# Performance work log

Measured on AMD Instinct MI355X. Metric: run time of the kernel, lower is better.

Reference implementation:

```python
import jax, jax.numpy as jnp
import numpy as np

NEG = -1e30


def _layernorm(x, g, b, eps=1e-6):
    mu = jnp.mean(x, axis=-1, keepdims=True)
    var = jnp.mean((x - mu) ** 2, axis=-1, keepdims=True)
    return (x - mu) * jax.lax.rsqrt(var + eps) * g + b


def _ctc_loss(log_probs, targets, input_lengths, target_lengths, blank):
    # log_probs: (T, B, V); targets: (B, L) int; lengths: (B,) int
    T, B, V = log_probs.shape
    L = targets.shape[1]
    S = 2 * L + 1
    # extended target sequence: blank, t0, blank, t1, ..., blank
    ext = jnp.full((B, S), blank, dtype=targets.dtype)
    ext = ext.at[:, 1::2].set(targets)
    # skip transition allowed where label differs from label two back and is not blank
    ext_m2 = jnp.pad(ext, ((0, 0), (2, 0)), constant_values=blank)[:, :S]
    skip_mask = (jnp.arange(S)[None, :] >= 2) & (ext != ext_m2) & (ext != blank)
    # gather per-step emission log-probs for extended labels: (T, B, S)
    lp_ext = jnp.take_along_axis(
        log_probs, jnp.broadcast_to(ext[None], (T, B, S)), axis=2
    )

    alpha0 = jnp.full((B, S), NEG, dtype=log_probs.dtype)
    alpha0 = alpha0.at[:, 0].set(lp_ext[0, :, 0])
    alpha0 = alpha0.at[:, 1].set(lp_ext[0, :, 1])

    def step(alpha, lp_e):
        a1 = jnp.pad(alpha, ((0, 0), (1, 0)), constant_values=NEG)[:, :S]
        a2 = jnp.pad(alpha, ((0, 0), (2, 0)), constant_values=NEG)[:, :S]
        a2 = jnp.where(skip_mask, a2, NEG)
        new = jnp.logaddexp(jnp.logaddexp(alpha, a1), a2) + lp_e
        return new, new

    _, alphas_rest = jax.lax.scan(step, alpha0, lp_ext[1:])
    alphas = jnp.concatenate([alpha0[None], alphas_rest], axis=0)  # (T, B, S)

    alpha_T = alphas[input_lengths - 1, jnp.arange(B)]  # (B, S)
    s_end = 2 * target_lengths  # final blank position
    l_blank = jnp.take_along_axis(alpha_T, s_end[:, None], axis=1)[:, 0]
    l_label = jnp.take_along_axis(alpha_T, (s_end - 1)[:, None], axis=1)[:, 0]
    loss_b = -jnp.logaddexp(l_blank, l_label)
    # zero_infinity=True
    loss_b = jnp.where(loss_b > 1e29, 0.0, loss_b)
    # reduction='mean': divide each loss by its target length, then batch-mean
    return jnp.mean(loss_b / target_lengths.astype(loss_b.dtype))


def setup_inputs() -> dict:
    T, B, D, V, L = 2000, 32, 768, 1024, 150
    key = jax.random.key(0)
    ks = jax.random.split(key, 8)
    s = 0.02
    return {
        "source_encoder_output": jax.random.normal(ks[0], (T, B, D), jnp.float32),
        "W_proj": jax.random.normal(ks[1], (D, D), jnp.float32) * s,
        "b_proj": jnp.zeros((D,), jnp.float32),
        "W_tr": jax.random.normal(ks[2], (D, D), jnp.float32) * s,
        "b_tr": jnp.zeros((D,), jnp.float32),
        "ln_g": jnp.ones((D,), jnp.float32),
        "ln_b": jnp.zeros((D,), jnp.float32),
        "W_dec": jax.random.normal(ks[3], (D, V), jnp.float32) * s,
        "b_dec": jnp.zeros((V,), jnp.float32),
        "target_syllabe_ids": jax.random.randint(ks[4], (B, L), 1, V, jnp.int32),
        "source_encoder_output_lengths": jnp.full((B,), T, jnp.int32),
        "target_syllabe_id_lengths": jnp.full((B,), L, jnp.int32),
    }


def reference(source_encoder_output, W_proj, b_proj, W_tr, b_tr, ln_g, ln_b,
              W_dec, b_dec, target_syllabe_ids, source_encoder_output_lengths,
              target_syllabe_id_lengths):
    BLANK = 0
    x = source_encoder_output @ W_proj + b_proj          # encoder_projection
    x = jax.nn.gelu(x @ W_tr + b_tr, approximate=False)  # transform dense + gelu
    x = _layernorm(x, ln_g, ln_b, eps=1e-6)
    scores = x @ W_dec + b_dec                           # acoustic_decoder
    log_probs = jax.nn.log_softmax(scores, axis=-1)      # (T, B, V)
    return _ctc_loss(log_probs, target_syllabe_ids,
                     source_encoder_output_lengths,
                     target_syllabe_id_lengths, BLANK)
```

## Files before the change

### kernel.cpp

```cpp
#include <hip/hip_runtime.h>
#include <hip/hip_bf16.h>
#include <math.h>
#include <stdint.h>

#define NEGF (-1e30f)
#define LOG2E 1.44269504088896340736f
#define LN2 0.69314718055994530942f

#define LPROW 512

typedef short bf16x8 __attribute__((ext_vector_type(8)));
typedef float f32x4 __attribute__((ext_vector_type(4)));

__device__ __forceinline__ unsigned short f2b(float x) {
  __hip_bfloat16 h = __float2bfloat16(x);
  return *reinterpret_cast<unsigned short*>(&h);
}
__device__ __forceinline__ float b2f(unsigned short u) {
  __hip_bfloat16 h;
  *reinterpret_cast<unsigned short*>(&h) = u;
  return __bfloat162float(h);
}
__device__ __forceinline__ float gelu_exact(float x) {
  return 0.5f * x * (1.0f + erff(x * 0.70710678118654752440f));
}

#if __has_builtin(__builtin_amdgcn_logf)
__device__ __forceinline__ float fast_log2(float x) { return __builtin_amdgcn_logf(x); }
#else
__device__ __forceinline__ float fast_log2(float x) { return log2f(x); }
#endif

template<int CTRL>
__device__ __forceinline__ float dpp_shr(float x) {
  return __int_as_float(__builtin_amdgcn_update_dpp(
      0, __float_as_int(x), 0x110 | CTRL, 0xf, 0xf, true));
}
__device__ __forceinline__ float readlane_f(float x, int l) {
  return __int_as_float(__builtin_amdgcn_readlane(__float_as_int(x), l));
}

__device__ __forceinline__ void gload16(void* lds, const void* g) {
  __builtin_amdgcn_global_load_lds(
      (__attribute__((address_space(1))) void*)(uintptr_t)g,
      (__attribute__((address_space(3))) void*)(unsigned int)(uintptr_t)lds,
      16, 0, 0);
}

__global__ __launch_bounds__(256) void cvt_enc_kernel(
    const float* __restrict__ in, unsigned short* __restrict__ out, long n4)
{
  long i = (long)blockIdx.x * blockDim.x + threadIdx.x;
  const long stride = (long)gridDim.x * blockDim.x;
  for (; i < n4; i += stride) {
    float4 v = ((const float4*)in)[i];
    ushort4 o;
    o.x = f2b(v.x); o.y = f2b(v.y); o.z = f2b(v.z); o.w = f2b(v.w);
    ((ushort4*)out)[i] = o;
  }
}

__global__ __launch_bounds__(256) void cvt_wt_kernel(
    const float* __restrict__ W, unsigned short* __restrict__ WT, int K, int N)
{
  __shared__ float tile[32][33];
  const int n0 = blockIdx.x * 32, k0 = blockIdx.y * 32;
  const int tx = threadIdx.x, ty = threadIdx.y;
#pragma unroll
  for (int i = 0; i < 32; i += 8) {
    int k = k0 + ty + i, n = n0 + tx;
    tile[ty + i][tx] = (k < K && n < N) ? W[(long)k * N + n] : 0.f;
  }
  __syncthreads();
#pragma unroll
  for (int i = 0; i < 32; i += 8) {
    int n = n0 + ty + i, k = k0 + tx;
    if (n < N && k < K) WT[(long)n * K + k] = f2b(tile[tx][ty + i]);
  }
}

template<int NFULL, int EPI>
__global__ __launch_bounds__(256, 2) void gemm128_kernel(
    const unsigned short* __restrict__ A,
    const unsigned short* __restrict__ WT,
    const float* __restrict__ bias,
    unsigned short* __restrict__ out,
    float2* __restrict__ partials,
    int K)
{
  extern __shared__ char smem[];
  unsigned short* As = (unsigned short*)smem;
  unsigned short* Bs = (unsigned short*)(smem + 16384);

  const int tid = threadIdx.x, lane = tid & 63, w = tid >> 6;
  const int wr = w >> 1, wc = w & 1;
  const int cl = lane & 15, g = lane >> 4;
  const int bx = blockIdx.x;
  const long row0 = (long)blockIdx.y * 128;
  const int col0 = bx * 128;

  const int ch0 = w * 64 + lane;
  const int ch1 = 256 + ch0;
  const unsigned short* Ag0 = A + (row0 + (ch0 >> 2)) * K + (ch0 & 3) * 8;
  const unsigned short* Ag1 = A + (row0 + (ch1 >> 2)) * K + (ch1 & 3) * 8;
  const unsigned short* Bg0 = WT + (long)(col0 + (ch0 >> 2)) * K + (ch0 & 3) * 8;
  const unsigned short* Bg1 = WT + (long)(col0 + (ch1 >> 2)) * K + (ch1 & 3) * 8;
  unsigned short* Al0 = As + w * 512;
  unsigned short* Al1 = As + 2048 + w * 512;
  unsigned short* Bl0 = Bs + w * 512;
  unsigned short* Bl1 = Bs + 2048 + w * 512;

#define STAGE(buf, kt)                          \
  do {                                          \
    const int _ko = (kt) * 32;                  \
    gload16(Al0 + (buf) * 4096, Ag0 + _ko);     \
    gload16(Al1 + (buf) * 4096, Ag1 + _ko);     \
    gload16(Bl0 + (buf) * 4096, Bg0 + _ko);     \
    gload16(Bl1 + (buf) * 4096, Bg1 + _ko);     \
  } while (0)

  f32x4 acc[4][4];
#pragma unroll
  for (int mt = 0; mt < 4; ++mt)
#pragma unroll
    for (int nt = 0; nt < 4; ++nt) acc[mt][nt] = (f32x4){0.f, 0.f, 0.f, 0.f};

  const int NKT = K / 32;
  STAGE(0, 0);
  __syncthreads();
  int buf = 0;
  for (int kt = 0; kt < NKT; ++kt) {
    if (kt + 1 < NKT) STAGE(buf ^ 1, kt + 1);
    const unsigned short* Ab = As + buf * 4096;
    const unsigned short* Bb = Bs + buf * 4096;
    bf16x8 af[4], bfr[4];
#pragma unroll
    for (int mt = 0; mt < 4; ++mt)
      af[mt] = *(const bf16x8*)&Ab[(((wr * 64 + mt * 16 + cl) << 2) + g) * 8];
#pragma unroll
    for (int nt = 0; nt < 4; ++nt)
      bfr[nt] = *(const bf16x8*)&Bb[(((wc * 64 + nt * 16 + cl) << 2) + g) * 8];
#pragma unroll
    for (int mt = 0; mt < 4; ++mt)
#pragma unroll
      for (int nt = 0; nt < 4; ++nt)
        acc[mt][nt] = __builtin_amdgcn_mfma_f32_16x16x32_bf16(
            af[mt], bfr[nt], acc[mt][nt], 0, 0, 0);
    __syncthreads();
    buf ^= 1;
  }
#undef STAGE

  float bv[4];
#pragma unroll
  for (int nt = 0; nt < 4; ++nt) bv[nt] = bias[col0 + wc * 64 + nt * 16 + cl];
#pragma unroll
  for (int mt = 0; mt < 4; ++mt)
#pragma unroll
    for (int nt = 0; nt < 4; ++nt)
#pragma unroll
      for (int j = 0; j < 4; ++j) {
        float v = acc[mt][nt][j] + bv[nt];
        if (EPI == 1) v = gelu_exact(v);
        acc[mt][nt][j] = v;
      }

  if (EPI == 2) {
#pragma unroll
    for (int mt = 0; mt < 4; ++mt)
#pragma unroll
      for (int j = 0; j < 4; ++j) {
        float mx = fmaxf(fmaxf(acc[mt][0][j], acc[mt][1][j]),
                         fmaxf(acc[mt][2][j], acc[mt][3][j]));
#pragma unroll
        for (int off = 1; off < 16; off <<= 1)
          mx = fmaxf(mx, __shfl_xor(mx, off));
        float sm = 0.f;
#pragma unroll
        for (int nt = 0; nt < 4; ++nt) sm += expf(acc[mt][nt][j] - mx);
#pragma unroll
        for (int off = 1; off < 16; off <<= 1) sm += __shfl_xor(sm, off);
        if (cl == 0) {
          long m = row0 + wr * 64 + mt * 16 + g * 4 + j;
          partials[m * 16 + bx * 2 + wc] = make_float2(mx, sm);
        }
      }
  }

  unsigned short* Ct = (unsigned short*)smem;
#pragma unroll
  for (int mt = 0; mt < 4; ++mt)
#pragma unroll
    for (int nt = 0; nt < 4; ++nt)
#pragma unroll
      for (int j = 0; j < 4; ++j)
        Ct[(wr * 64 + mt * 16 + g * 4 + j) * 136 + wc * 64 + nt * 16 + cl] =
            f2b(acc[mt][nt][j]);
  __syncthreads();
  for (int idx = tid; idx < 2048; idx += 256) {
    int r = idx >> 4, ch = idx & 15;
    *(bf16x8*)&out[(row0 + r) * NFULL + col0 + ch * 8] =
        *(const bf16x8*)&Ct[r * 136 + ch * 8];
  }
}

template<int D>
__global__ __launch_bounds__(256) void ln_bf16_kernel(
    unsigned short* __restrict__ X, const float* __restrict__ g,
    const float* __restrict__ bt, long M)
{
  constexpr int NI = D / 256;
  const int lane = threadIdx.x & 63;
  const int wid = threadIdx.x >> 6;
  const long row = (long)blockIdx.x * 4 + wid;
  if (row >= M) return;

  float v[NI * 4];
  float s = 0.f;
#pragma unroll
  for (int i = 0; i < NI; ++i) {
    ushort4 u = *(const ushort4*)&X[row * D + (i * 64 + lane) * 4];
    v[i * 4 + 0] = b2f(u.x); v[i * 4 + 1] = b2f(u.y);
    v[i * 4 + 2] = b2f(u.z); v[i * 4 + 3] = b2f(u.w);
    s += v[i * 4 + 0] + v[i * 4 + 1] + v[i * 4 + 2] + v[i * 4 + 3];
  }
#pragma unroll
  for (int off = 32; off; off >>= 1) s += __shfl_xor(s, off);
  const float mu = s * (1.0f / D);
  float q = 0.f;
#pragma unroll
  for (int i = 0; i < NI * 4; ++i) { float d = v[i] - mu; q += d * d; }
#pragma unroll
  for (int off = 32; off; off >>= 1) q += __shfl_xor(q, off);
  const float rs = rsqrtf(q * (1.0f / D) + 1e-6f);
#pragma unroll
  for (int i = 0; i < NI; ++i) {
    ushort4 o;
    int c = (i * 64 + lane) * 4;
    o.x = f2b((v[i * 4 + 0] - mu) * rs * g[c + 0] + bt[c + 0]);
    o.y = f2b((v[i * 4 + 1] - mu) * rs * g[c + 1] + bt[c + 1]);
    o.z = f2b((v[i * 4 + 2] - mu) * rs * g[c + 2] + bt[c + 2]);
    o.w = f2b((v[i * 4 + 3] - mu) * rs * g[c + 3] + bt[c + 3]);
    *(ushort4*)&X[row * D + c] = o;
  }
}

__global__ __launch_bounds__(256) void logz_gather_kernel(
    const unsigned short* __restrict__ scores,
    const float2* __restrict__ partials,
    const int* __restrict__ targets,
    unsigned short* __restrict__ lp_ext,
    long Mtot, int T, int B, int L, int S)
{
  const int w = threadIdx.x >> 6, lane = threadIdx.x & 63;
  const long m = (long)blockIdx.x * 4 + w;
  if (m >= Mtot) return;

  float2 pp = partials[m * 16 + (lane & 15)];
  float Mx = pp.x, Sv = pp.y;
#pragma unroll
  for (int off = 1; off < 16; off <<= 1) {
    float Mo = __shfl_xor(Mx, off);
    float So = __shfl_xor(Sv, off);
    float Mn = fmaxf(Mx, Mo);
    Sv = Sv * expf(Mx - Mn) + So * expf(Mo - Mn);
    Mx = Mn;
  }
  const float logz = Mx + logf(Sv);
  const int b = (int)(m % B);
  const int t = (int)(m / B);
  const unsigned short* srow = scores + m * 1024;
  bf16x8 o = {0, 0, 0, 0, 0, 0, 0, 0};
#pragma unroll
  for (int j = 0; j < 5; ++j) {
    int s = lane * 5 + j;
    if (s < S) {
      int lab = (s & 1) ? targets[b * L + (s >> 1)] : 0;
      o[j] = (short)f2b(expf(b2f(srow[lab]) - logz) * 1024.0f);
    }
  }
  *(bf16x8*)&lp_ext[((long)b * T + t) * LPROW + lane * 8] = o;
}

#define CHUNK 32
__global__ __launch_bounds__(256, 1) void ctc_scan_kernel(
    const unsigned short* __restrict__ pr,
    const int* __restrict__ targets, const int* __restrict__ inlens,
    const int* __restrict__ tlens, float* __restrict__ partial,
    int T, int B, int L, int S)
{
  extern __shared__ char smem[];
  unsigned short* ring = (unsigned short*)smem;

  const int b = blockIdx.x;
  const int tid = threadIdx.x;
  const int lane = tid & 63;
  const int w = tid >> 6;
  const int s0 = lane * 5;
  const int inlen = inlens[b];
  const int tlen = tlens[b];
  const int send = 2 * tlen;
  const int capT = inlen - 1;
  const bool is16 = (lane == 16), is32 = (lane == 32), is48 = (lane == 48);

  const unsigned short* pbase = pr + (long)b * T * LPROW;

  float skm[5];
#pragma unroll
  for (int j = 0; j < 5; ++j) {
    int s = s0 + j;
    float sk = 0.f;
    if (s < S && (s & 1) && s >= 3) {
      int lab = targets[b * L + (s >> 1)];
      int lab2 = targets[b * L + (s >> 1) - 1];
      sk = ((lab != 0) && (lab != lab2)) ? 1.f : 0.f;
    }
    skm[j] = sk;
  }

  float a[5];
  float abv = 0.f, alv = 0.f;
  int corr = 0, corr_cap = 0;
#pragma unroll
  for (int j = 0; j < 5; ++j) {
    int s = s0 + j;
    a[j] = (s <= 1) ? b2f(pbase[lane * 8 + j]) : 0.f;
  }
  if (capT == 0) {
#pragma unroll
    for (int j = 0; j < 5; ++j) {
      int s = s0 + j;
      if (s == send) abv = a[j];
      if (s == send - 1) alv = a[j];
    }
    corr_cap = corr;
  }

#define STAGE_CHUNK(bf, t0)                                                   \
  do {                                                                        \
    _Pragma("unroll")                                                         \
    for (int s_ = 0; s_ < 8; ++s_) {                                          \
      const int r_ = s_ * 4 + w;                                              \
      if ((t0) + r_ < T)                                                      \
        gload16(ring + (bf) * 16384 + r_ * 512,                               \
                pbase + ((long)(t0) + r_) * 512 + lane * 8);                  \
    }                                                                         \
  } while (0)

#define CTC_PROCESS(vv, tcur)                                                 \
  do {                                                                        \
    float p_[5];                                                              \
    _Pragma("unroll")                                                         \
    for (int j = 0; j < 5; ++j) p_[j] = b2f((unsigned short)(vv)[j]);         \
    float r15 = readlane_f(a[4], 15), r31 = readlane_f(a[4], 31),             \
          r47 = readlane_f(a[4], 47);                                         \
    float q15 = readlane_f(a[3], 15), q31 = readlane_f(a[3], 31),             \
          q47 = readlane_f(a[3], 47);                                         \
    float o_m1 = dpp_shr<1>(a[4]);                                            \
    float o_m2 = dpp_shr<1>(a[3]);                                            \
    o_m1 = is16 ? r15 : o_m1; o_m1 = is32 ? r31 : o_m1;                       \
    o_m1 = is48 ? r47 : o_m1;                                                 \
    o_m2 = is16 ? q15 : o_m2; o_m2 = is32 ? q31 : o_m2;                       \
    o_m2 = is48 ? q47 : o_m2;                                                 \
    float na0 = fmaf(skm[0], o_m2, a[0] + o_m1) * p_[0];                      \
    float na1 = fmaf(skm[1], o_m1, a[1] + a[0]) * p_[1];                      \
    float na2 = fmaf(skm[2], a[0], a[2] + a[1]) * p_[2];                      \
    float na3 = fmaf(skm[3], a[1], a[3] + a[2]) * p_[3];                      \
    float na4 = fmaf(skm[4], a[2], a[4] + a[3]) * p_[4];                      \
    a[0] = na0; a[1] = na1; a[2] = na2; a[3] = na3; a[4] = na4;               \
    if ((tcur) == capT) {                                                     \
      _Pragma("unroll")                                                       \
      for (int j = 0; j < 5; ++j) {                                           \
        int s = s0 + j;                                                       \
        if (s == send) abv = a[j];                                            \
        if (s == send - 1) alv = a[j];                                        \
      }                                                                       \
      corr_cap = corr;                                                        \
    }                                                                         \
  } while (0)

#define CTC_RENORM                                                            \
  do {                                                                        \
    float m_ = fmaxf(fmaxf(fmaxf(a[0], a[1]), fmaxf(a[2], a[3])), a[4]);      \
    m_ = fmaxf(m_, dpp_shr<1>(m_));                                           \
    m_ = fmaxf(m_, dpp_shr<2>(m_));                                           \
    m_ = fmaxf(m_, dpp_shr<4>(m_));                                           \
    m_ = fmaxf(m_, dpp_shr<8>(m_));                                           \
    float mx = fmaxf(fmaxf(readlane_f(m_, 15), readlane_f(m_, 31)),           \
                     fmaxf(readlane_f(m_, 47), readlane_f(m_, 63)));          \
    int e;                                                                    \
    (void)frexpf(mx, &e);                      \
    float sc = ldexpf(1.f, -e);                                               \
    _Pragma("unroll")                                                         \
    for (int j = 0; j < 5; ++j) a[j] *= sc;                                   \
    corr += e;                                                                \
  } while (0)

  const int nch = (T + CHUNK - 1) / CHUNK;
  STAGE_CHUNK(0, 0);
  __syncthreads();
  int buf = 0;
  for (int c = 0; c < nch; ++c) {
    if (c + 1 < nch) STAGE_CHUNK(buf ^ 1, (c + 1) * CHUNK);
    if (w == 0) {
      const unsigned short* rb = ring + buf * 16384 + lane * 8;
      const int t0 = c * CHUNK;
      bf16x8 vv[4];
      vv[0] = *(const bf16x8*)&rb[0 * 512];
      vv[1] = *(const bf16x8*)&rb[1 * 512];
      vv[2] = *(const bf16x8*)&rb[2 * 512];
#pragma unroll
      for (int r = 0; r < CHUNK; ++r) {
        if (r + 3 < CHUNK) vv[(r + 3) & 3] = *(const bf16x8*)&rb[(r + 3) * 512];
        const int t = t0 + r;
        if (t >= 1 && t < T) CTC_PROCESS(vv[r & 3], t);
        if ((r & 7) == 7) CTC_RENORM;
      }
    }
    __syncthreads();
    buf ^= 1;
  }

  if (w == 0) {
#pragma unroll
    for (int off = 32; off; off >>= 1) {
      abv = fmaxf(abv, __shfl_xor(abv, off));
      alv = fmaxf(alv, __shfl_xor(alv, off));
    }
    if (lane == 0) {
      float l2 = fast_log2(abv + alv) + (float)corr_cap - 10.0f * (float)inlen;
      float loss = -LN2 * l2;
      if (!(loss <= 1e29f)) loss = 0.f;
      partial[b] = loss / (float)tlen;
    }
  }
}

__global__ void reduce_kernel(const float* __restrict__ partial,
                              float* __restrict__ out, int B)
{
  int lane = threadIdx.x;
  float v = (lane < B) ? partial[lane] : 0.f;
#pragma unroll
  for (int off = 32; off; off >>= 1) v += __shfl_xor(v, off);
  if (lane == 0) out[0] = v / (float)B;
}

extern "C" void kernel_launch(void* const* d_in, const int* in_sizes, int n_in,
                              void* d_out, int out_size, void* d_ws, size_t ws_size,
                              hipStream_t stream) {
  const float* enc = (const float*)d_in[0];
  const float* Wp  = (const float*)d_in[1];
  const float* bp  = (const float*)d_in[2];
  const float* Wt  = (const float*)d_in[3];
  const float* btr = (const float*)d_in[4];
  const float* lng = (const float*)d_in[5];
  const float* lnb = (const float*)d_in[6];
  const float* Wd  = (const float*)d_in[7];
  const float* bd  = (const float*)d_in[8];
  const int* tgt   = (const int*)d_in[9];
  const int* inl   = (const int*)d_in[10];
  const int* tll   = (const int*)d_in[11];

  const int D = in_sizes[2];
  const int V = in_sizes[8];
  const int B = in_sizes[10];
  const int L = in_sizes[9] / B;
  const long M = (long)in_sizes[0] / D;
  const int T = (int)(M / B);
  const int S = 2 * L + 1;

  char* wsb = (char*)d_ws;
  size_t off = 0;
  auto alloc = [&](size_t bytes) { char* p = wsb + off; off += (bytes + 255) & ~(size_t)255; return p; };
  unsigned short* encb   = (unsigned short*)alloc((size_t)M * D * 2);
  char* x1region         = alloc((size_t)M * V * 2);
  unsigned short* X1b    = (unsigned short*)x1region;
  unsigned short* scores = (unsigned short*)x1region;
  unsigned short* X2b    = encb;
  unsigned short* LP     = (unsigned short*)alloc((size_t)B * T * LPROW * 2);
  float2* partials       = (float2*)alloc((size_t)M * 16 * sizeof(float2));
  unsigned short* WpT    = (unsigned short*)alloc((size_t)D * D * 2);
  unsigned short* WtT    = (unsigned short*)alloc((size_t)D * D * 2);
  unsigned short* WdT    = (unsigned short*)alloc((size_t)D * V * 2);
  float* partial         = (float*)alloc(256);

  cvt_wt_kernel<<<dim3(D / 32, D / 32), dim3(32, 8), 0, stream>>>(Wp, WpT, D, D);
  cvt_wt_kernel<<<dim3(D / 32, D / 32), dim3(32, 8), 0, stream>>>(Wt, WtT, D, D);
  cvt_wt_kernel<<<dim3(V / 32, D / 32), dim3(32, 8), 0, stream>>>(Wd, WdT, D, V);
  cvt_enc_kernel<<<2048, 256, 0, stream>>>(enc, encb, (long)M * D / 4);

  const size_t smemg = 34816;
  const dim3 g12(D / 128, (unsigned)(M / 128));
  const dim3 g3(V / 128, (unsigned)(M / 128));

  gemm128_kernel<768, 0><<<g12, 256, smemg, stream>>>(encb, WpT, bp, X1b, nullptr, D);
  gemm128_kernel<768, 1><<<g12, 256, smemg, stream>>>(X1b, WtT, btr, X2b, nullptr, D);
  ln_bf16_kernel<768><<<(int)(M / 4), 256, 0, stream>>>(X2b, lng, lnb, M);
  gemm128_kernel<1024, 2><<<g3, 256, smemg, stream>>>(X2b, WdT, bd, scores, partials, D);

  logz_gather_kernel<<<(int)(M / 4), 256, 0, stream>>>(
      scores, partials, tgt, LP, M, T, B, L, S);
  ctc_scan_kernel<<<B, 256, 65536, stream>>>(LP, tgt, inl, tll, partial, T, B, L, S);
  reduce_kernel<<<1, 64, 0, stream>>>(partial, (float*)d_out, B);
}
```

Measured before the change: 814.8 us.

## Replace LDS double-buffered CTC scan with single-wave register prefetch ring

New measurement: 806.9 us. Within noise of the previous version (-1.0%).

```diff
diff --git a/kernel.cpp b/kernel.cpp
--- a/kernel.cpp
+++ b/kernel.cpp
@@ -38,6 +38,12 @@
 }
 __device__ __forceinline__ float readlane_f(float x, int l) {
   return __int_as_float(__builtin_amdgcn_readlane(__float_as_int(x), l));
+}
+
+__device__ __forceinline__ uint4 gload_x4(const void* p) {
+  uint4 r;
+  asm volatile("global_load_dwordx4 %0, %1, off" : "=v"(r) : "v"(p));
+  return r;
 }
 
 __device__ __forceinline__ void gload16(void* lds, const void* g) {
@@ -282,20 +288,15 @@
   *(bf16x8*)&lp_ext[((long)b * T + t) * LPROW + lane * 8] = o;
 }
 
-#define CHUNK 32
-__global__ __launch_bounds__(256, 1) void ctc_scan_kernel(
+#define CTC_DEPTH 16
+__global__ __launch_bounds__(64, 1) void ctc_scan_kernel(
     const unsigned short* __restrict__ pr,
     const int* __restrict__ targets, const int* __restrict__ inlens,
     const int* __restrict__ tlens, float* __restrict__ partial,
     int T, int B, int L, int S)
 {
-  extern __shared__ char smem[];
-  unsigned short* ring = (unsigned short*)smem;
-
   const int b = blockIdx.x;
-  const int tid = threadIdx.x;
-  const int lane = tid & 63;
-  const int w = tid >> 6;
+  const int lane = threadIdx.x;
   const int s0 = lane * 5;
   const int inlen = inlens[b];
   const int tlen = tlens[b];
@@ -303,7 +304,7 @@
   const int capT = inlen - 1;
   const bool is16 = (lane == 16), is32 = (lane == 32), is48 = (lane == 48);
 
-  const unsigned short* pbase = pr + (long)b * T * LPROW;
+  const unsigned short* lpb = pr + (long)b * T * LPROW + lane * 8;
 
   float skm[5];
 #pragma unroll
@@ -324,7 +325,7 @@
 #pragma unroll
   for (int j = 0; j < 5; ++j) {
     int s = s0 + j;
-    a[j] = (s <= 1) ? b2f(pbase[lane * 8 + j]) : 0.f;
+    a[j] = (s <= 1) ? b2f(lpb[j]) : 0.f;
   }
   if (capT == 0) {
 #pragma unroll
@@ -336,22 +337,13 @@
     corr_cap = corr;
   }
 
-#define STAGE_CHUNK(bf, t0)                                                   \
+#define CTC_PROCESS(rd, tcur)                                                 \
   do {                                                                        \
-    _Pragma("unroll")                                                         \
-    for (int s_ = 0; s_ < 8; ++s_) {                                          \
-      const int r_ = s_ * 4 + w;                                              \
-      if ((t0) + r_ < T)                                                      \
-        gload16(ring + (bf) * 16384 + r_ * 512,                               \
-                pbase + ((long)(t0) + r_) * 512 + lane * 8);                  \
-    }                                                                         \
-  } while (0)
-
-#define CTC_PROCESS(vv, tcur)                                                 \
-  do {                                                                        \
-    float p_[5];                                                              \
-    _Pragma("unroll")                                                         \
-    for (int j = 0; j < 5; ++j) p_[j] = b2f((unsigned short)(vv)[j]);         \
+    float p0 = __uint_as_float((rd).x << 16);                                 \
+    float p1 = __uint_as_float((rd).x & 0xffff0000u);                         \
+    float p2 = __uint_as_float((rd).y << 16);                                 \
+    float p3 = __uint_as_float((rd).y & 0xffff0000u);                         \
+    float p4 = __uint_as_float((rd).z << 16);                                 \
     float r15 = readlane_f(a[4], 15), r31 = readlane_f(a[4], 31),             \
           r47 = readlane_f(a[4], 47);                                         \
     float q15 = readlane_f(a[3], 15), q31 = readlane_f(a[3], 31),             \
@@ -362,11 +354,11 @@
     o_m1 = is48 ? r47 : o_m1;                                                 \
     o_m2 = is16 ? q15 : o_m2; o_m2 = is32 ? q31 : o_m2;                       \
     o_m2 = is48 ? q47 : o_m2;                                                 \
-    float na0 = fmaf(skm[0], o_m2, a[0] + o_m1) * p_[0];                      \
-    float na1 = fmaf(skm[1], o_m1, a[1] + a[0]) * p_[1];                      \
-    float na2 = fmaf(skm[2], a[0], a[2] + a[1]) * p_[2];                      \
-    float na3 = fmaf(skm[3], a[1], a[3] + a[2]) * p_[3];                      \
-    float na4 = fmaf(skm[4], a[2], a[4] + a[3]) * p_[4];                      \
+    float na0 = fmaf(skm[0], o_m2, a[0] + o_m1) * p0;                         \
+    float na1 = fmaf(skm[1], o_m1, a[1] + a[0]) * p1;                         \
+    float na2 = fmaf(skm[2], a[0], a[2] + a[1]) * p2;                         \
+    float na3 = fmaf(skm[3], a[1], a[3] + a[2]) * p3;                         \
+    float na4 = fmaf(skm[4], a[2], a[4] + a[3]) * p4;                         \
     a[0] = na0; a[1] = na1; a[2] = na2; a[3] = na3; a[4] = na4;               \
     if ((tcur) == capT) {                                                     \
       _Pragma("unroll")                                                       \
@@ -396,43 +388,36 @@
     corr += e;                                                                \
   } while (0)
 
-  const int nch = (T + CHUNK - 1) / CHUNK;
-  STAGE_CHUNK(0, 0);
-  __syncthreads();
-  int buf = 0;
-  for (int c = 0; c < nch; ++c) {
-    if (c + 1 < nch) STAGE_CHUNK(buf ^ 1, (c + 1) * CHUNK);
-    if (w == 0) {
-      const unsigned short* rb = ring + buf * 16384 + lane * 8;
-      const int t0 = c * CHUNK;
-      bf16x8 vv[4];
-      vv[0] = *(const bf16x8*)&rb[0 * 512];
-      vv[1] = *(const bf16x8*)&rb[1 * 512];
-      vv[2] = *(const bf16x8*)&rb[2 * 512];
-#pragma unroll
-      for (int r = 0; r < CHUNK; ++r) {
-        if (r + 3 < CHUNK) vv[(r + 3) & 3] = *(const bf16x8*)&rb[(r + 3) * 512];
-        const int t = t0 + r;
-        if (t >= 1 && t < T) CTC_PROCESS(vv[r & 3], t);
-        if ((r & 7) == 7) CTC_RENORM;
-      }
+  uint4 ring[CTC_DEPTH];
+#pragma unroll
+  for (int d = 0; d < CTC_DEPTH; ++d)
+    ring[d] = gload_x4(lpb + (long)(1 + d) * LPROW);
+
+  const int NCH = (T - 1 + CTC_DEPTH - 1) / CTC_DEPTH;
+  int t = 1;
+  for (int c = 0; c < NCH; ++c) {
+#pragma unroll
+    for (int d = 0; d < CTC_DEPTH; ++d) {
+      asm volatile("s_waitcnt vmcnt(15)" ::: "memory");
+      __builtin_amdgcn_sched_barrier(0);
+      if (t < T) CTC_PROCESS(ring[d], t);
+      ring[d] = gload_x4(lpb + (long)(t + CTC_DEPTH) * LPROW);
+      if ((d & 7) == 7) CTC_RENORM;
+      ++t;
     }
-    __syncthreads();
-    buf ^= 1;
-  }
-
-  if (w == 0) {
-#pragma unroll
-    for (int off = 32; off; off >>= 1) {
-      abv = fmaxf(abv, __shfl_xor(abv, off));
-      alv = fmaxf(alv, __shfl_xor(alv, off));
-    }
-    if (lane == 0) {
-      float l2 = fast_log2(abv + alv) + (float)corr_cap - 10.0f * (float)inlen;
-      float loss = -LN2 * l2;
-      if (!(loss <= 1e29f)) loss = 0.f;
-      partial[b] = loss / (float)tlen;
-    }
+  }
+  asm volatile("s_waitcnt vmcnt(0)" ::: "memory");
+
+#pragma unroll
+  for (int off = 32; off; off >>= 1) {
+    abv = fmaxf(abv, __shfl_xor(abv, off));
+    alv = fmaxf(alv, __shfl_xor(alv, off));
+  }
+  if (lane == 0) {
+    float l2 = fast_log2(abv + alv) + (float)corr_cap - 10.0f * (float)inlen;
+    float loss = -LN2 * l2;
+    if (!(loss <= 1e29f)) loss = 0.f;
+    partial[b] = loss / (float)tlen;
   }
 }
 
@@ -478,7 +463,7 @@
   unsigned short* X1b    = (unsigned short*)x1region;
   unsigned short* scores = (unsigned short*)x1region;
   unsigned short* X2b    = encb;
-  unsigned short* LP     = (unsigned short*)alloc((size_t)B * T * LPROW * 2);
+  unsigned short* LP     = (unsigned short*)alloc((size_t)B * T * LPROW * 2 + 65536);
   float2* partials       = (float2*)alloc((size_t)M * 16 * sizeof(float2));
   unsigned short* WpT    = (unsigned short*)alloc((size_t)D * D * 2);
   unsigned short* WtT    = (unsigned short*)alloc((size_t)D * D * 2);
@@ -501,6 +486,6 @@
 
   logz_gather_kernel<<<(int)(M / 4), 256, 0, stream>>>(
       scores, partials, tgt, LP, M, T, B, L, S);
-  ctc_scan_kernel<<<B, 256, 65536, stream>>>(LP, tgt, inl, tll, partial, T, B, L, S);
+  ctc_scan_kernel<<<B, 64, 0, stream>>>(LP, tgt, inl, tll, partial, T, B, L, S);
   reduce_kernel<<<1, 64, 0, stream>>>(partial, (float*)d_out, B);
 }
```
